# Kernel tuning notes

Hardware: AMD Instinct MI355X
Metric: run time of the kernel (lower is better)

## Reference

```python
import jax, jax.numpy as jnp
import numpy as np

EMBED_DIM = 1024


def setup_inputs() -> dict:
    key = jax.random.key(0)
    ks = jax.random.split(key, 7)
    B, S, D = 4, 2048, EMBED_DIM
    scale = 1.0 / np.sqrt(D)
    x = jax.random.normal(ks[0], (B, S, D), dtype=jnp.float32)
    # nn.Linear weights stored as [out, in]; we keep [in, out] for x @ W
    Wq = jax.random.normal(ks[1], (D, D), dtype=jnp.float32) * scale
    bq = jax.random.normal(ks[2], (D,), dtype=jnp.float32) * scale
    Wk = jax.random.normal(ks[3], (D, D), dtype=jnp.float32) * scale
    bk = jax.random.normal(ks[4], (D,), dtype=jnp.float32) * scale
    Wv = jax.random.normal(ks[5], (D, D), dtype=jnp.float32) * scale
    bv = jax.random.normal(ks[6], (D,), dtype=jnp.float32) * scale
    return {"x": x, "Wq": Wq, "bq": bq, "Wk": Wk, "bk": bk, "Wv": Wv, "bv": bv}


def reference(x, Wq, bq, Wk, bk, Wv, bv):
    # Single-head attention (num_heads unused in original module).
    q = x @ Wq + bq            # [B, S, D]
    k = x @ Wk + bk            # [B, S, D]
    v = x @ Wv + bv            # [B, S, D]
    inv_sqrt_d = 1.0 / jnp.sqrt(jnp.asarray(x.shape[-1], x.dtype))
    scores = jnp.einsum("bsd,btd->bst", q, k) * inv_sqrt_d  # [B, S, S]
    attn = jax.nn.softmax(scores, axis=-1)
    return jnp.einsum("bst,btd->bsd", attn, v)
```

## Files before the change

### kernel.cpp

```cpp
#include <hip/hip_runtime.h>
#include <hip/hip_bf16.h>


using floatx4 = __attribute__((ext_vector_type(4))) float;
using shortx8 = __attribute__((ext_vector_type(8))) short;
using shortx4 = __attribute__((ext_vector_type(4))) short;

__device__ __forceinline__ short f2bf(float f) {
    __hip_bfloat16 h = __float2bfloat16(f);
    return *reinterpret_cast<short*>(&h);
}
__device__ __forceinline__ float bf2f(short s) {
    unsigned u = (unsigned)(unsigned short)s << 16;
    return __uint_as_float(u);
}

#define MFMA16(a, b, c) __builtin_amdgcn_mfma_f32_16x16x32_bf16((a), (b), (c), 0, 0, 0)

__device__ __forceinline__ void gld_lds16(const void* g, void* l) {
    __builtin_amdgcn_global_load_lds(
        (const __attribute__((address_space(1))) void*)g,
        (__attribute__((address_space(3))) void*)l, 16, 0, 0);
}

template<int MH>
__device__ __forceinline__ void rdA(const short* sAb, int wm, int lrow,
                                    int xo0, int xo1, shortx8 (&af)[4][2]) {
    const short* base = sAb + ((wm << 7) + (MH << 6) + lrow) * 64;
#pragma unroll
    for (int i = 0; i < 4; ++i) {
        af[i][0] = *reinterpret_cast<const shortx8*>(base + i * 1024 + xo0);
        af[i][1] = *reinterpret_cast<const shortx8*>(base + i * 1024 + xo1);
    }
}
template<int NH>
__device__ __forceinline__ void rdB(const short* sBb, int wn, int lrow,
                                    int xo0, int xo1, shortx8 (&bf)[4][2]) {
    const short* base = sBb + ((wn << 6) + (NH << 5) + lrow) * 64;
#pragma unroll
    for (int j = 0; j < 2; ++j) {
        bf[NH * 2 + j][0] = *reinterpret_cast<const shortx8*>(base + j * 1024 + xo0);
        bf[NH * 2 + j][1] = *reinterpret_cast<const shortx8*>(base + j * 1024 + xo1);
    }
}
template<int MH, int NH>
__device__ __forceinline__ void mfq(shortx8 (&af)[4][2], shortx8 (&bf)[4][2],
                                    floatx4 (&acc)[8][4]) {
    __builtin_amdgcn_s_setprio(1);
#pragma unroll
    for (int i = 0; i < 4; ++i) {
#pragma unroll
        for (int j = 0; j < 2; ++j) {
            acc[MH * 4 + i][NH * 2 + j] =
                MFMA16(af[i][0], bf[NH * 2 + j][0], acc[MH * 4 + i][NH * 2 + j]);
            acc[MH * 4 + i][NH * 2 + j] =
                MFMA16(af[i][1], bf[NH * 2 + j][1], acc[MH * 4 + i][NH * 2 + j]);
        }
    }
    __builtin_amdgcn_s_setprio(0);
}

__device__ __forceinline__ void gemm256_loop8(
    const short* __restrict__ A, const short* __restrict__ B,
    int lda, int ldb, int K,
    short* sA, short* sB, floatx4 (&acc)[8][4], int t)
{
    const int w = t >> 6, l = t & 63;
    const int wm = w >> 2, wn = w & 3;
    const int lrow = l & 15, quad = l >> 4, r8 = lrow & 7;
    const int xo0 = (quad ^ r8) << 3;
    const int xo1 = ((quad + 4) ^ r8) << 3;
    const int rr = t >> 3;
    const int gsw = ((t & 7) ^ (rr & 7)) << 3;
    const short* gA0 = A + (size_t)rr * lda + gsw;
    const short* gA1 = A + (size_t)(128 + rr) * lda + gsw;
    const short* gB0 = B + (size_t)rr * ldb + gsw;
    const short* gB1 = B + (size_t)(128 + rr) * ldb + gsw;
    const int wofs = w << 9;

    auto stage = [&](const short* g, int ld, int kt, short* ldsb) {
        const short* p = g + kt;
        gld_lds16(p, ldsb + wofs);
        gld_lds16(p + (size_t)(ld << 6), ldsb + wofs + 4096);
    };

    shortx8 af[4][2], bf[4][2];
    const int NT = K >> 6;

    stage(gA0, lda, 0, sA);
    stage(gA1, lda, 0, sA + 8192);
    stage(gB0, ldb, 0, sB);
    stage(gB1, ldb, 0, sB + 8192);
    stage(gB0, ldb, 64, sB + 16384);
    stage(gB1, ldb, 64, sB + 16384 + 8192);
    asm volatile("s_waitcnt vmcnt(4)" ::: "memory");
    __builtin_amdgcn_s_barrier();

    for (int T = 0; T < NT; T += 2) {
        const bool more = (T + 2) < NT;
        const int ktA1 = (T + 1) << 6;
        const int ktN2 = (T + 2) << 6;
        const int ktB3 = (T + 3) << 6;
        short* sA0 = sA;           short* sB0 = sB;
        short* sA1 = sA + 16384;   short* sB1 = sB + 16384;

        rdA<0>(sA0, wm, lrow, xo0, xo1, af);
        rdB<0>(sB0, wn, lrow, xo0, xo1, bf);
        stage(gA0, lda, ktA1, sA1);
        asm volatile("s_waitcnt lgkmcnt(8)" ::: "memory");
        __builtin_amdgcn_s_barrier();
        asm volatile("s_waitcnt lgkmcnt(0)" ::: "memory");
        __builtin_amdgcn_sched_barrier(0);
        mfq<0, 0>(af, bf, acc);
        __builtin_amdgcn_s_barrier();
        rdB<1>(sB0, wn, lrow, xo0, xo1, bf);
        stage(gA1, lda, ktA1, sA1 + 8192);
        __builtin_amdgcn_s_barrier();
        asm volatile("s_waitcnt lgkmcnt(0)" ::: "memory");
        __builtin_amdgcn_sched_barrier(0);
        mfq<0, 1>(af, bf, acc);
        __builtin_amdgcn_s_barrier();
        rdA<1>(sA0, wm, lrow, xo0, xo1, af);
        if (more) stage(gB0, ldb, ktN2, sB0);
        __builtin_amdgcn_s_barrier();
        asm volatile("s_waitcnt lgkmcnt(0)" ::: "memory");
        __builtin_amdgcn_sched_barrier(0);
        mfq<1, 0>(af, bf, acc);
        __builtin_amdgcn_s_barrier();
        if (more) stage(gB1, ldb, ktN2, sB0 + 8192);
        __builtin_amdgcn_s_barrier();
        __builtin_amdgcn_sched_barrier(0);
        mfq<1, 1>(af, bf, acc);
        if (more) { asm volatile("s_waitcnt vmcnt(4)" ::: "memory"); }
        else      { asm volatile("s_waitcnt vmcnt(0)" ::: "memory"); }
        __builtin_amdgcn_s_barrier();

        rdA<0>(sA1, wm, lrow, xo0, xo1, af);
        rdB<0>(sB1, wn, lrow, xo0, xo1, bf);
        if (more) stage(gA0, lda, ktN2, sA0);
        asm volatile("s_waitcnt lgkmcnt(8)" ::: "memory");
        __builtin_amdgcn_s_barrier();
        asm volatile("s_waitcnt lgkmcnt(0)" ::: "memory");
        __builtin_amdgcn_sched_barrier(0);
        mfq<0, 0>(af, bf, acc);
        __builtin_amdgcn_s_barrier();
        rdB<1>(sB1, wn, lrow, xo0, xo1, bf);
        if (more) stage(gA1, lda, ktN2, sA0 + 8192);
        __builtin_amdgcn_s_barrier();
        asm volatile("s_waitcnt lgkmcnt(0)" ::: "memory");
        __builtin_amdgcn_sched_barrier(0);
        mfq<0, 1>(af, bf, acc);
        __builtin_amdgcn_s_barrier();
        rdA<1>(sA1, wm, lrow, xo0, xo1, af);
        if (more) stage(gB0, ldb, ktB3, sB1);
        __builtin_amdgcn_s_barrier();
        asm volatile("s_waitcnt lgkmcnt(0)" ::: "memory");
        __builtin_amdgcn_sched_barrier(0);
        mfq<1, 0>(af, bf, acc);
        __builtin_amdgcn_s_barrier();
        if (more) stage(gB1, ldb, ktB3, sB1 + 8192);
        __builtin_amdgcn_s_barrier();
        __builtin_amdgcn_sched_barrier(0);
        mfq<1, 1>(af, bf, acc);
        if (more) { asm volatile("s_waitcnt vmcnt(4)" ::: "memory"); }
        __builtin_amdgcn_s_barrier();
    }
}

__device__ __forceinline__ void gemm_loop(
    const short* __restrict__ A, const short* __restrict__ B,
    size_t lda, size_t ldb, int K,
    short* as_, short* bs_, floatx4 (&acc)[4][4], int w, int l)
{
    const int lr8 = l >> 3;
    const int swz = ((l & 7) ^ lr8) * 8;
    const int lrow = l & 15, quad = l >> 4;
    const int wr = w >> 1, wc = w & 1;
    const int r8r = lrow & 7;
    const short* pa = A + (size_t)(w * 32 + lr8) * lda + swz;
    const short* pb = B + (size_t)(w * 32 + lr8) * ldb + swz;
    short* la = as_ + w * 4 * 512;
    short* lb = bs_ + w * 4 * 512;

    for (int kt = 0; kt < K; kt += 64) {
        for (int c = 0; c < 4; ++c) {
            gld_lds16(pa + (size_t)c * 8 * lda + kt, la + c * 512);
            gld_lds16(pb + (size_t)c * 8 * ldb + kt, lb + c * 512);
        }
        __syncthreads();
        for (int kk = 0; kk < 64; kk += 32) {
            const int xoff = (((kk >> 3) + quad) ^ r8r) << 3;
            shortx8 af[4], bfr[4];
            for (int i = 0; i < 4; ++i)
                af[i] = *reinterpret_cast<const shortx8*>(
                    &as_[(size_t)(wr * 64 + i * 16 + lrow) * 64 + xoff]);
            for (int j = 0; j < 4; ++j)
                bfr[j] = *reinterpret_cast<const shortx8*>(
                    &bs_[(size_t)(wc * 64 + j * 16 + lrow) * 64 + xoff]);
            for (int i = 0; i < 4; ++i)
                for (int j = 0; j < 4; ++j)
                    acc[i][j] = MFMA16(af[i], bfr[j], acc[i][j]);
        }
        __syncthreads();
    }
}

__global__ __launch_bounds__(256) void prep_kernel(
    const float* __restrict__ X,
    const float* __restrict__ Wq, const float* __restrict__ Wk,
    const float* __restrict__ Wv,
    const float* __restrict__ bq, const float* __restrict__ bk,
    const float* __restrict__ bv,
    short* __restrict__ Xb, short* __restrict__ Wt,
    float* __restrict__ bcat)
{
    const int id = blockIdx.x, t = threadIdx.x;
    if (id < 4096) {
        size_t i = ((size_t)id * 256 + t) * 8;
        float4 v0 = *reinterpret_cast<const float4*>(X + i);
        float4 v1 = *reinterpret_cast<const float4*>(X + i + 4);
        shortx8 s;
        s[0] = f2bf(v0.x); s[1] = f2bf(v0.y); s[2] = f2bf(v0.z); s[3] = f2bf(v0.w);
        s[4] = f2bf(v1.x); s[5] = f2bf(v1.y); s[6] = f2bf(v1.z); s[7] = f2bf(v1.w);
        *reinterpret_cast<shortx8*>(Xb + i) = s;
    } else if (id < 4864) {
        __shared__ float tl[64][65];
        const int wid = id - 4096;
        const int z = wid >> 8, t16 = wid & 255;
        const float* src = (z == 0) ? Wq : (z == 1) ? Wk : Wv;
        short* dst = Wt + (size_t)z * 1024 * 1024;
        const int k0 = (t16 >> 4) * 64, n0 = (t16 & 15) * 64;
        for (int i = t; i < 64 * 64; i += 256) {
            int r = i >> 6, c = i & 63;
            tl[r][c] = src[(size_t)(k0 + r) * 1024 + n0 + c];
        }
        __syncthreads();
        for (int i = t; i < 64 * 64; i += 256) {
            int r = i >> 6, c = i & 63;
            dst[(size_t)(n0 + r) * 1024 + k0 + c] = f2bf(tl[c][r]);
        }
    } else {
        const int z = id - 4864;
        const float* bsrc = (z == 0) ? bq : (z == 1) ? bk : bv;
        for (int i = t; i < 1024; i += 256) bcat[z * 1024 + i] = bsrc[i];
    }
}

__global__ __launch_bounds__(512, 2) void qkv_qk_kernel(
    const short* __restrict__ Xb, const short* __restrict__ Wt,
    const float* __restrict__ bcat, short* __restrict__ dQ,
    short* __restrict__ dK)
{
    __shared__ short sA[2 * 16384];
    __shared__ short sB[2 * 16384];
    const int t = threadIdx.x;
    const int m0 = blockIdx.x * 256, n0 = blockIdx.y * 256;
    const int w = t >> 6, l = t & 63;
    const int wm = w >> 2, wn = w & 3, lrow = l & 15, quad = l >> 4;
    const int sec = n0 >> 10;

    floatx4 acc[8][4];
#pragma unroll
    for (int i = 0; i < 8; ++i)
#pragma unroll
        for (int j = 0; j < 4; ++j) acc[i][j] = floatx4{0.f, 0.f, 0.f, 0.f};

    gemm256_loop8(Xb + (size_t)m0 * 1024, Wt + (size_t)n0 * 1024,
                  1024, 1024, 1024, sA, sB, acc, t);

    short* outN = (sec == 0) ? dQ : dK;
#pragma unroll
    for (int i = 0; i < 8; ++i) {
        int rbase = m0 + wm * 128 + i * 16 + quad * 4;
#pragma unroll
        for (int j = 0; j < 4; ++j) {
            int coln = n0 + wn * 64 + j * 16 + lrow;
            int col = coln & 1023;
            float bvv = bcat[coln];
#pragma unroll
            for (int r = 0; r < 4; ++r)
                outN[(size_t)(rbase + r) * 1024 + col] =
                    f2bf(acc[i][j][r] + bvv);
        }
    }
}

__global__ __launch_bounds__(256) void qkv_v_kernel(
    const short* __restrict__ Xb, const short* __restrict__ Wt,
    const float* __restrict__ bcat, short* __restrict__ Vt)
{
    __shared__ short as_[128 * 64];
    __shared__ short bs_[128 * 64];
    const int t = threadIdx.x, w = t >> 6, l = t & 63;
    const int m0 = blockIdx.x * 128;
    const int n0 = 2048 + blockIdx.y * 128;
    const int wr = w >> 1, wc = w & 1, lrow = l & 15, quad = l >> 4;

    floatx4 acc[4][4];
    for (int i = 0; i < 4; ++i)
        for (int j = 0; j < 4; ++j) acc[i][j] = floatx4{0.f, 0.f, 0.f, 0.f};

    gemm_loop(Xb + (size_t)m0 * 1024, Wt + (size_t)n0 * 1024,
              1024, 1024, 1024, as_, bs_, acc, w, l);

    for (int i = 0; i < 4; ++i) {
        int rbase = m0 + wr * 64 + i * 16 + quad * 4;
        int b = rbase >> 11, sl = rbase & 2047;
        for (int j = 0; j < 4; ++j) {
            int coln = n0 + wc * 64 + j * 16 + lrow;
            int col = coln & 1023;
            float bvv = bcat[coln];
            shortx4 s;
            for (int r = 0; r < 4; ++r) s[r] = f2bf(acc[i][j][r] + bvv);
            *reinterpret_cast<shortx4*>(
                &Vt[((size_t)b * 1024 + col) * 2048 + sl]) = s;
        }
    }
}

__global__ __launch_bounds__(512, 2) void scores_kernel(
    const short* __restrict__ dQ, const short* __restrict__ dK,
    short* __restrict__ P, float* __restrict__ partials, int row_start)
{
    __shared__ short sA[2 * 16384];
    __shared__ short sB[2 * 16384];
    const int t = threadIdx.x;
    int bx = blockIdx.x, by = blockIdx.y;
    if (gridDim.x == 32) {
        const int c = bx & 7;
        const int k = (bx >> 3) + (by << 2);
        const int bb = c >> 1, half = c & 1;
        bx = bb * 8 + (k & 3) + 4 * half;
        by = k >> 2;
    }
    const int m0 = bx * 256;
    const int n0 = by * 256;
    const int g0 = row_start + m0;
    const int b = g0 >> 11;
    const int w = t >> 6, l = t & 63;
    const int wm = w >> 2, wn = w & 3, lrow = l & 15, quad = l >> 4;

    floatx4 acc[8][4];
#pragma unroll
    for (int i = 0; i < 8; ++i)
#pragma unroll
        for (int j = 0; j < 4; ++j) acc[i][j] = floatx4{0.f, 0.f, 0.f, 0.f};

    gemm256_loop8(dQ + (size_t)g0 * 1024, dK + ((size_t)b * 2048 + n0) * 1024,
                  1024, 1024, 1024, sA, sB, acc, t);

    float* sred = reinterpret_cast<float*>(sA);
#pragma unroll
    for (int i = 0; i < 8; ++i) {
        int rl = wm * 128 + i * 16 + quad * 4;
        int rloc = m0 + rl;
        float rs[4] = {0.f, 0.f, 0.f, 0.f};
#pragma unroll
        for (int j = 0; j < 4; ++j) {
            int col = n0 + wn * 64 + j * 16 + lrow;
#pragma unroll
            for (int r = 0; r < 4; ++r) {
                short pb = f2bf(__expf(acc[i][j][r] * 0.03125f - 20.0f));
                P[(size_t)(rloc + r) * 2048 + col] = pb;
                rs[r] += bf2f(pb);
            }
        }
#pragma unroll
        for (int r = 0; r < 4; ++r)
            for (int m = 1; m <= 8; m <<= 1)
                rs[r] += __shfl_xor(rs[r], m, 64);
        if (lrow == 0)
#pragma unroll
            for (int r = 0; r < 4; ++r)
                sred[(rl + r) * 4 + wn] = rs[r];
    }
    __syncthreads();
    if (t < 256) {
        float s = sred[t * 4] + sred[t * 4 + 1] + sred[t * 4 + 2] + sred[t * 4 + 3];
        partials[(size_t)(row_start + m0 + t) * 8 + by] = s;
    }
}

__global__ __launch_bounds__(256) void pv_kernel(
    const short* __restrict__ P, const short* __restrict__ Vt,
    const float* __restrict__ partials, float* __restrict__ Out, int row_start)
{
    __shared__ short as_[128 * 64];
    __shared__ short bs_[128 * 64];
    const int t = threadIdx.x, w = t >> 6, l = t & 63;
    int bx = blockIdx.x, by = blockIdx.y;
    if (gridDim.x == 64) {
        const int c = bx & 7;
        const int k = (bx >> 3) + (by << 3);
        const int bb = c >> 1, half = c & 1;
        bx = bb * 16 + (k & 7) + 8 * half;
        by = k >> 3;
    }
    const int m0 = bx * 128;
    const int n0 = by * 128;
    const int g0 = row_start + m0;
    const int b = g0 >> 11;
    const int wr = w >> 1, wc = w & 1, lrow = l & 15, quad = l >> 4;

    floatx4 acc[4][4];
    for (int i = 0; i < 4; ++i)
        for (int j = 0; j < 4; ++j) acc[i][j] = floatx4{0.f, 0.f, 0.f, 0.f};

    gemm_loop(P + (size_t)m0 * 2048, Vt + ((size_t)b * 1024 + n0) * 2048,
              2048, 2048, 2048, as_, bs_, acc, w, l);

    for (int i = 0; i < 4; ++i) {
        int rloc = m0 + wr * 64 + i * 16 + quad * 4;
        int rglb = row_start + rloc;
        float is[4];
        for (int r = 0; r < 4; ++r) {
            const float4* pp =
                reinterpret_cast<const float4*>(&partials[(size_t)(rglb + r) * 8]);
            float4 p0 = pp[0], p1 = pp[1];
            float s = (p0.x + p0.y) + (p0.z + p0.w) +
                      (p1.x + p1.y) + (p1.z + p1.w);
            is[r] = 1.0f / s;
        }
        for (int j = 0; j < 4; ++j) {
            int col = n0 + wc * 64 + j * 16 + lrow;
            for (int r = 0; r < 4; ++r)
                Out[(size_t)(rglb + r) * 1024 + col] = acc[i][j][r] * is[r];
        }
    }
}

extern "C" void kernel_launch(void* const* d_in, const int* in_sizes, int n_in,
                              void* d_out, int out_size, void* d_ws, size_t ws_size,
                              hipStream_t stream)
{
    const float* x  = (const float*)d_in[0];
    const float* Wq = (const float*)d_in[1];
    const float* bq = (const float*)d_in[2];
    const float* Wk = (const float*)d_in[3];
    const float* bk = (const float*)d_in[4];
    const float* Wv = (const float*)d_in[5];
    const float* bv = (const float*)d_in[6];
    float* out = (float*)d_out;

    short* dQ = (short*)d_out;
    short* dK = dQ + (size_t)8192 * 1024;

    char* ws = (char*)d_ws;
    short* Wt   = (short*)ws;
    float* bcat = (float*)(ws + 6291456);
    float* partials = (float*)(ws + 6291456 + 12288);
    short* Vt   = (short*)(ws + 6291456 + 12288 + 262144);
    char*  region = ws + 6291456 + 12288 + 262144 + 16777216;
    const size_t base = 6291456 + 12288 + 262144 + 16777216;

    size_t avail = ws_size > base ? ws_size - base : 0;
    long rows_fit = (long)(avail / 4096);
    int chunk = (int)(rows_fit & ~255L);
    if (chunk > 8192) chunk = 8192;
    if (chunk < 256) chunk = 256;
    short* Xb = (short*)region;
    short* P  = (short*)region;

    prep_kernel<<<dim3(4867), 256, 0, stream>>>(x, Wq, Wk, Wv, bq, bk, bv,
                                                Xb, Wt, bcat);
    qkv_qk_kernel<<<dim3(32, 8), 512, 0, stream>>>(Xb, Wt, bcat, dQ, dK);
    qkv_v_kernel<<<dim3(64, 8), 256, 0, stream>>>(Xb, Wt, bcat, Vt);

    for (int rs = 0; rs < 8192; rs += chunk) {
        int rows = 8192 - rs;
        if (rows > chunk) rows = chunk;
        scores_kernel<<<dim3(rows / 256, 8), 512, 0, stream>>>(dQ, dK, P, partials, rs);
        pv_kernel<<<dim3(rows / 128, 8), 256, 0, stream>>>(P, Vt, partials, out, rs);
    }
}
```

Baseline: 230.4 us.

## Retile PV GEMM to 256x128 blocks with 8 waves and double-buffered LDS pipeline

The P·V kernel moves from 128x128 tiles with 4 waves to 256x128 tiles with 8 waves. It uses a new double-buffered direct-to-LDS pipeline modeled on the scores kernel, with staged loads interleaved between MFMA phases and setprio around the MFMA groups. The grid swizzle is adjusted for the smaller grid. The larger tile improves reuse of the V operand and reduces the number of blocks. In exchange it uses more LDS per block (96KB), which may limit occupancy, and the grid is smaller at 256 blocks.

```diff
diff --git a/kernel.cpp b/kernel.cpp
--- a/kernel.cpp
+++ b/kernel.cpp
@@ -113,6 +113,7 @@
         __builtin_amdgcn_sched_barrier(0);
         mfq<0, 0>(af, bf, acc);
         __builtin_amdgcn_s_barrier();
+
         rdB<1>(sB0, wn, lrow, xo0, xo1, bf);
         stage(gA1, lda, ktA1, sA1 + 8192);
         __builtin_amdgcn_s_barrier();
@@ -120,6 +121,7 @@
         __builtin_amdgcn_sched_barrier(0);
         mfq<0, 1>(af, bf, acc);
         __builtin_amdgcn_s_barrier();
+
         rdA<1>(sA0, wm, lrow, xo0, xo1, af);
         if (more) stage(gB0, ldb, ktN2, sB0);
         __builtin_amdgcn_s_barrier();
@@ -127,6 +129,7 @@
         __builtin_amdgcn_sched_barrier(0);
         mfq<1, 0>(af, bf, acc);
         __builtin_amdgcn_s_barrier();
+
         if (more) stage(gB1, ldb, ktN2, sB0 + 8192);
         __builtin_amdgcn_s_barrier();
         __builtin_amdgcn_sched_barrier(0);
@@ -144,6 +147,7 @@
         __builtin_amdgcn_sched_barrier(0);
         mfq<0, 0>(af, bf, acc);
         __builtin_amdgcn_s_barrier();
+
         rdB<1>(sB1, wn, lrow, xo0, xo1, bf);
         if (more) stage(gA1, lda, ktN2, sA0 + 8192);
         __builtin_amdgcn_s_barrier();
@@ -151,6 +155,7 @@
         __builtin_amdgcn_sched_barrier(0);
         mfq<0, 1>(af, bf, acc);
         __builtin_amdgcn_s_barrier();
+
         rdA<1>(sA1, wm, lrow, xo0, xo1, af);
         if (more) stage(gB0, ldb, ktB3, sB1);
         __builtin_amdgcn_s_barrier();
@@ -158,11 +163,118 @@
         __builtin_amdgcn_sched_barrier(0);
         mfq<1, 0>(af, bf, acc);
         __builtin_amdgcn_s_barrier();
+
         if (more) stage(gB1, ldb, ktB3, sB1 + 8192);
         __builtin_amdgcn_s_barrier();
         __builtin_amdgcn_sched_barrier(0);
         mfq<1, 1>(af, bf, acc);
         if (more) { asm volatile("s_waitcnt vmcnt(4)" ::: "memory"); }
+        __builtin_amdgcn_s_barrier();
+    }
+}
+
+__device__ __forceinline__ void rdB2(const short* sBb, int wn, int lrow,
+                                     int xo0, int xo1, shortx8 (&bf)[2][2]) {
+    const short* base = sBb + ((wn << 5) + lrow) * 64;
+#pragma unroll
+    for (int j = 0; j < 2; ++j) {
+        bf[j][0] = *reinterpret_cast<const shortx8*>(base + j * 1024 + xo0);
+        bf[j][1] = *reinterpret_cast<const shortx8*>(base + j * 1024 + xo1);
+    }
+}
+template<int MH>
+__device__ __forceinline__ void mfqA(shortx8 (&af)[4][2], shortx8 (&bf)[2][2],
+                                     floatx4 (&acc)[8][2]) {
+    __builtin_amdgcn_s_setprio(1);
+#pragma unroll
+    for (int i = 0; i < 4; ++i) {
+#pragma unroll
+        for (int j = 0; j < 2; ++j) {
+            acc[MH * 4 + i][j] = MFMA16(af[i][0], bf[j][0], acc[MH * 4 + i][j]);
+            acc[MH * 4 + i][j] = MFMA16(af[i][1], bf[j][1], acc[MH * 4 + i][j]);
+        }
+    }
+    __builtin_amdgcn_s_setprio(0);
+}
+
+__device__ __forceinline__ void gemm256x128_loop(
+    const short* __restrict__ A, const short* __restrict__ B,
+    int lda, int ldb, int K,
+    short* sA, short* sB, floatx4 (&acc)[8][2], int t)
+{
+    const int w = t >> 6, l = t & 63;
+    const int wm = w >> 2, wn = w & 3;
+    const int lrow = l & 15, quad = l >> 4, r8 = lrow & 7;
+    const int xo0 = (quad ^ r8) << 3;
+    const int xo1 = ((quad + 4) ^ r8) << 3;
+    const int rr = t >> 3;
+    const int gsw = ((t & 7) ^ (rr & 7)) << 3;
+    const short* gA0 = A + (size_t)rr * lda + gsw;
+    const short* gA1 = A + (size_t)(128 + rr) * lda + gsw;
+    const short* gB0 = B + (size_t)rr * ldb + gsw;
+    const int wofs = w << 9;
+
+    auto stage = [&](const short* g, int ld, int kt, short* ldsb) {
+        const short* p = g + kt;
+        gld_lds16(p, ldsb + wofs);
+        gld_lds16(p + (size_t)(ld << 6), ldsb + wofs + 4096);
+    };
+
+    shortx8 af[4][2], bf[2][2];
+    const int NT = K >> 6;
+    short* sA0 = sA;           short* sB0 = sB;
+    short* sA1 = sA + 16384;   short* sB1 = sB + 8192;
+
+    stage(gA0, lda, 0, sA0); stage(gA1, lda, 0, sA0 + 8192);
+    stage(gB0, ldb, 0, sB0);
+    stage(gA0, lda, 64, sA1); stage(gA1, lda, 64, sA1 + 8192);
+    stage(gB0, ldb, 64, sB1);
+    asm volatile("s_waitcnt vmcnt(6)" ::: "memory");
+    __builtin_amdgcn_s_barrier();
+
+    for (int T = 0; T < NT; T += 2) {
+        const bool m2 = (T + 2) < NT;
+        const int ktA1 = (T + 1) << 6;
+        const int kt2  = (T + 2) << 6;
+        const int kt3  = (T + 3) << 6;
+
+        rdA<0>(sA0, wm, lrow, xo0, xo1, af);
+        rdB2(sB0, wn, lrow, xo0, xo1, bf);
+        if (T > 0) { stage(gA0, lda, ktA1, sA1); stage(gA1, lda, ktA1, sA1 + 8192); }
+        asm volatile("s_waitcnt lgkmcnt(8)" ::: "memory");
+        __builtin_amdgcn_s_barrier();
+        asm volatile("s_waitcnt lgkmcnt(0)" ::: "memory");
+        __builtin_amdgcn_sched_barrier(0);
+        mfqA<0>(af, bf, acc);
+        __builtin_amdgcn_s_barrier();
+
+        rdA<1>(sA0, wm, lrow, xo0, xo1, af);
+        if (m2) stage(gB0, ldb, kt2, sB0);
+        __builtin_amdgcn_s_barrier();
+        asm volatile("s_waitcnt lgkmcnt(0)" ::: "memory");
+        __builtin_amdgcn_sched_barrier(0);
+        mfqA<1>(af, bf, acc);
+        if (m2) { asm volatile("s_waitcnt vmcnt(2)" ::: "memory"); }
+        else    { asm volatile("s_waitcnt vmcnt(0)" ::: "memory"); }
+        __builtin_amdgcn_s_barrier();
+
+        rdA<0>(sA1, wm, lrow, xo0, xo1, af);
+        rdB2(sB1, wn, lrow, xo0, xo1, bf);
+        if (m2) { stage(gA0, lda, kt2, sA0); stage(gA1, lda, kt2, sA0 + 8192); }
+        asm volatile("s_waitcnt lgkmcnt(8)" ::: "memory");
+        __builtin_amdgcn_s_barrier();
+        asm volatile("s_waitcnt lgkmcnt(0)" ::: "memory");
+        __builtin_amdgcn_sched_barrier(0);
+        mfqA<0>(af, bf, acc);
+        __builtin_amdgcn_s_barrier();
+
+        rdA<1>(sA1, wm, lrow, xo0, xo1, af);
+        if (m2) stage(gB0, ldb, kt3, sB1);
+        __builtin_amdgcn_s_barrier();
+        asm volatile("s_waitcnt lgkmcnt(0)" ::: "memory");
+        __builtin_amdgcn_sched_barrier(0);
+        mfqA<1>(af, bf, acc);
+        if (m2) { asm volatile("s_waitcnt vmcnt(2)" ::: "memory"); }
         __builtin_amdgcn_s_barrier();
     }
 }
@@ -381,38 +493,43 @@
     }
 }
 
-__global__ __launch_bounds__(256) void pv_kernel(
+__global__ __launch_bounds__(512, 2) void pv_kernel(
     const short* __restrict__ P, const short* __restrict__ Vt,
     const float* __restrict__ partials, float* __restrict__ Out, int row_start)
 {
-    __shared__ short as_[128 * 64];
-    __shared__ short bs_[128 * 64];
-    const int t = threadIdx.x, w = t >> 6, l = t & 63;
+    __shared__ short sA[2 * 16384];
+    __shared__ short sB[2 * 8192];
+    const int t = threadIdx.x;
     int bx = blockIdx.x, by = blockIdx.y;
-    if (gridDim.x == 64) {
+    if (gridDim.x == 32) {
         const int c = bx & 7;
-        const int k = (bx >> 3) + (by << 3);
+        const int k = (bx >> 3) + (by << 2);
         const int bb = c >> 1, half = c & 1;
-        bx = bb * 16 + (k & 7) + 8 * half;
-        by = k >> 3;
-    }
-    const int m0 = bx * 128;
+        bx = bb * 8 + (k & 3) + 4 * half;
+        by = k >> 2;
+    }
+    const int m0 = bx * 256;
     const int n0 = by * 128;
     const int g0 = row_start + m0;
     const int b = g0 >> 11;
-    const int wr = w >> 1, wc = w & 1, lrow = l & 15, quad = l >> 4;
-
-    floatx4 acc[4][4];
-    for (int i = 0; i < 4; ++i)
-        for (int j = 0; j < 4; ++j) acc[i][j] = floatx4{0.f, 0.f, 0.f, 0.f};
-
-    gemm_loop(P + (size_t)m0 * 2048, Vt + ((size_t)b * 1024 + n0) * 2048,
-              2048, 2048, 2048, as_, bs_, acc, w, l);
-
-    for (int i = 0; i < 4; ++i) {
-        int rloc = m0 + wr * 64 + i * 16 + quad * 4;
-        int rglb = row_start + rloc;
+    const int w = t >> 6, l = t & 63;
+    const int wm = w >> 2, wn = w & 3, lrow = l & 15, quad = l >> 4;
+
+    floatx4 acc[8][2];
+#pragma unroll
+    for (int i = 0; i < 8; ++i)
+#pragma unroll
+        for (int j = 0; j < 2; ++j) acc[i][j] = floatx4{0.f, 0.f, 0.f, 0.f};
+
+    gemm256x128_loop(P + (size_t)m0 * 2048, Vt + ((size_t)b * 1024 + n0) * 2048,
+                     2048, 2048, 2048, sA, sB, acc, t);
+
+#pragma unroll
+    for (int ii = 0; ii < 8; ++ii) {
+        int rl = wm * 128 + (ii >> 2) * 64 + (ii & 3) * 16 + quad * 4;
+        int rglb = row_start + m0 + rl;
         float is[4];
+#pragma unroll
         for (int r = 0; r < 4; ++r) {
             const float4* pp =
                 reinterpret_cast<const float4*>(&partials[(size_t)(rglb + r) * 8]);
@@ -421,10 +538,12 @@
                       (p1.x + p1.y) + (p1.z + p1.w);
             is[r] = 1.0f / s;
         }
-        for (int j = 0; j < 4; ++j) {
-            int col = n0 + wc * 64 + j * 16 + lrow;
+#pragma unroll
+        for (int j = 0; j < 2; ++j) {
+            int col = n0 + wn * 32 + j * 16 + lrow;
+#pragma unroll
             for (int r = 0; r < 4; ++r)
-                Out[(size_t)(rglb + r) * 1024 + col] = acc[i][j][r] * is[r];
+                Out[(size_t)(rglb + r) * 1024 + col] = acc[ii][j][r] * is[r];
         }
     }
 }
@@ -470,6 +589,6 @@
         int rows = 8192 - rs;
         if (rows > chunk) rows = chunk;
         scores_kernel<<<dim3(rows / 256, 8), 512, 0, stream>>>(dQ, dK, P, partials, rs);
-        pv_kernel<<<dim3(rows / 128, 8), 256, 0, stream>>>(P, Vt, partials, out, rs);
-    }
-}
+        pv_kernel<<<dim3(rows / 256, 8), 512, 0, stream>>>(P, Vt, partials, out, rs);
+    }
+}
```

Measured after the change: 233.7 us. No clear change (+1.4%).
